# Kernel tuning notes

Hardware: AMD Instinct MI355X
Metric: run time of the kernel (lower is better)

Reference implementation:

```python
import jax, jax.numpy as jnp
import numpy as np

T, H, E, K, I = 4096, 1024, 8, 2, 2048
EPS = 1e-5


def setup_inputs() -> dict:
    key = jax.random.key(0)
    ks = jax.random.split(key, 5)
    xavier = jax.nn.initializers.variance_scaling(1.0, 'fan_avg', 'uniform', dtype=jnp.float32)
    return {
        'x': jax.random.normal(ks[0], (T, H), dtype=jnp.float32),
        'scale': jnp.ones((H,), dtype=jnp.float32),
        'gate_kernel': xavier(ks[1], (H, E), jnp.float32),
        'gate_bias': jnp.zeros((E,), dtype=jnp.float32),
        'mlp1_weight': xavier(ks[2], (E, 2 * I, H), jnp.float32),
        'mlp1_bias': jnp.zeros((E, 2 * I), dtype=jnp.float32),
        'mlp2_weight': xavier(ks[3], (E, H, I), jnp.float32),
        'mlp2_bias': jnp.zeros((E, H), dtype=jnp.float32),
    }


def reference(x, scale, gate_kernel, gate_bias, mlp1_weight, mlp1_bias, mlp2_weight, mlp2_bias):
    # RMSNorm in fp32
    t = x.astype(jnp.float32)
    rms = jnp.sqrt(jnp.mean(t * t, axis=-1, keepdims=True) + EPS)
    normed = ((t / rms) * scale).astype(x.dtype)  # [T, H]

    # Gating: top-k experts + softmax over selected logits
    gate_logits = normed @ gate_kernel + gate_bias  # [T, E]
    expert_logits, expert_indices = jax.lax.top_k(gate_logits, K)  # [T, K]
    expert_weights = jax.nn.softmax(expert_logits, axis=-1)  # [T, K]

    # Dense all-expert SwiGLU MLP (faithful to vmap-over-experts original)
    # mlp1_weight: [E, 2I, H] -> mlp1: [E, T, 2I]
    mlp1 = jnp.einsum('td,efd->etf', normed, mlp1_weight) + mlp1_bias[:, None, :]
    gate_part = jnp.minimum(mlp1[..., :I], 7.0)
    linear_part = jnp.clip(mlp1[..., I:], -7.0, 7.0)
    swish_gate = gate_part * jax.nn.sigmoid(1.702 * gate_part)
    activated = swish_gate * (linear_part + 1.0)  # [E, T, I]
    # mlp2_weight: [E, H, I] -> expert_outputs: [T, E, H]
    expert_outputs = (jnp.einsum('eti,ehi->eth', activated, mlp2_weight)
                      + mlp2_bias[:, None, :]).transpose(1, 0, 2)

    # Scatter top-k weights to dense [T, E] and combine
    one_hot = jax.nn.one_hot(expert_indices, E, dtype=expert_outputs.dtype)  # [T, K, E]
    dense_gate_weights = jnp.sum(one_hot * expert_weights[..., None], axis=1)  # [T, E]
    fused = jnp.einsum('teh,te->th', expert_outputs, dense_gate_weights)
    return x + fused
```

## Files before the change

kernel.cpp:

```cpp
#include <hip/hip_runtime.h>
#include <hip/hip_bf16.h>
#include <math.h>

#define T_ 4096
#define H_ 1024
#define E_ 8
#define KTOP 2
#define I_ 2048
#define EPS_ 1e-5f
#define LDST 72

using bf16x8 = __attribute__((ext_vector_type(8))) short;
using f32x4  = __attribute__((ext_vector_type(4))) float;

static __device__ __forceinline__ unsigned short f2bf(float f) {
    union { float f; unsigned int u; } v; v.f = f;
    unsigned int u = v.u;
    u += 0x7fffu + ((u >> 16) & 1u);
    return (unsigned short)(u >> 16);
}

__global__ __launch_bounds__(256) void k_norm_gate(
    const float* __restrict__ x, const float* __restrict__ scale,
    const float* __restrict__ gk, const float* __restrict__ gb,
    unsigned short* __restrict__ normed_bf,
    int* __restrict__ counts, int* __restrict__ tok_list, float* __restrict__ w_list)
{
    int t = blockIdx.x;
    int tid = threadIdx.x;
    int lane = tid & 63, wave = tid >> 6;

    float4 xv = ((const float4*)(x + (size_t)t * H_))[tid];
    float ss = xv.x*xv.x + xv.y*xv.y + xv.z*xv.z + xv.w*xv.w;
    #pragma unroll
    for (int off = 32; off; off >>= 1) ss += __shfl_down(ss, off);

    __shared__ float red[4];
    __shared__ float s_inv;
    if (lane == 0) red[wave] = ss;
    __syncthreads();
    if (tid == 0) {
        float tot = red[0] + red[1] + red[2] + red[3];
        s_inv = 1.0f / sqrtf(tot / (float)H_ + EPS_);
    }
    __syncthreads();
    float inv = s_inv;

    float4 sv = ((const float4*)scale)[tid];
    float nv[4];
    nv[0] = xv.x*inv*sv.x; nv[1] = xv.y*inv*sv.y;
    nv[2] = xv.z*inv*sv.z; nv[3] = xv.w*inv*sv.w;
    ushort4 nb;
    nb.x = f2bf(nv[0]); nb.y = f2bf(nv[1]); nb.z = f2bf(nv[2]); nb.w = f2bf(nv[3]);
    ((ushort4*)(normed_bf + (size_t)t * H_))[tid] = nb;

    float p[E_];
    #pragma unroll
    for (int e = 0; e < E_; e++) p[e] = 0.f;
    int h0 = tid * 4;
    #pragma unroll
    for (int j = 0; j < 4; j++) {
        const float4* g4 = (const float4*)(gk + (size_t)(h0 + j) * E_);
        float4 a = g4[0], b = g4[1];
        float n = nv[j];
        p[0] += n*a.x; p[1] += n*a.y; p[2] += n*a.z; p[3] += n*a.w;
        p[4] += n*b.x; p[5] += n*b.y; p[6] += n*b.z; p[7] += n*b.w;
    }
    __shared__ float pr[E_][4];
    #pragma unroll
    for (int e = 0; e < E_; e++) {
        float v = p[e];
        #pragma unroll
        for (int off = 32; off; off >>= 1) v += __shfl_down(v, off);
        if (lane == 0) pr[e][wave] = v;
    }
    __syncthreads();
    if (tid == 0) {
        float lg[E_];
        #pragma unroll
        for (int e = 0; e < E_; e++)
            lg[e] = pr[e][0] + pr[e][1] + pr[e][2] + pr[e][3] + gb[e];
        int b0 = -1, b1 = -1; float l0 = -1e30f, l1 = -1e30f;
        #pragma unroll
        for (int e = 0; e < E_; e++) {
            if (lg[e] > l0) { l1 = l0; b1 = b0; l0 = lg[e]; b0 = e; }
            else if (lg[e] > l1) { l1 = lg[e]; b1 = e; }
        }
        float e1 = expf(l1 - l0);
        float w0 = 1.f / (1.f + e1);
        float w1 = e1 / (1.f + e1);
        int p0 = atomicAdd(&counts[b0], 1);
        tok_list[b0 * T_ + p0] = t * 2 + 0; w_list[b0 * T_ + p0] = w0;
        int p1 = atomicAdd(&counts[b1], 1);
        tok_list[b1 * T_ + p1] = t * 2 + 1; w_list[b1 * T_ + p1] = w1;
    }
}

__global__ __launch_bounds__(256) void k_init_out(
    const float* __restrict__ x, float* __restrict__ out)
{
    size_t i = (size_t)blockIdx.x * 256 + threadIdx.x;
    ((float4*)out)[i] = ((const float4*)x)[i];
}

__global__ __launch_bounds__(256) void k_mlp1(
    const float* __restrict__ w1, const float* __restrict__ b1,
    const unsigned short* __restrict__ normed_bf,
    const int* __restrict__ counts, const int* __restrict__ tok_list,
    unsigned short* __restrict__ act)
{
    int e = blockIdx.z;
    int Ne = counts[e];
    int mt0 = blockIdx.y * 64;
    if (mt0 >= Ne) return;
    int it0 = blockIdx.x * 64;
    int tid = threadIdx.x;
    int lane = tid & 63, wave = tid >> 6;
    int quad = lane >> 4, m16 = lane & 15;

    __shared__ unsigned short lA[64 * LDST];
    __shared__ unsigned short lBg[64 * LDST];
    __shared__ unsigned short lBl[64 * LDST];
    __shared__ int ls_tk[64];

    if (tid < 64) {
        int slot = mt0 + tid;
        ls_tk[tid] = (slot < Ne) ? tok_list[e * T_ + slot] : -1;
    }
    __syncthreads();

    f32x4 accg[4], accl[4];
    #pragma unroll
    for (int ns = 0; ns < 4; ns++) {
        accg[ns] = (f32x4){0.f, 0.f, 0.f, 0.f};
        accl[ns] = (f32x4){0.f, 0.f, 0.f, 0.f};
    }

    const size_t w1base = (size_t)e * 2 * I_ * H_;
    int rA = tid >> 3, sgA = tid & 7;
    int nB = tid >> 2, sgB = tid & 3;

    for (int kk = 0; kk < H_; kk += 64) {
        #pragma unroll
        for (int rr = 0; rr < 64; rr += 32) {
            int r = rA + rr;
            int tk = ls_tk[r];
            uint4 v = make_uint4(0u, 0u, 0u, 0u);
            if (tk >= 0)
                v = *(const uint4*)(normed_bf + (size_t)(tk >> 1) * H_ + kk + sgA * 8);
            *(uint4*)(&lA[r * LDST + sgA * 8]) = v;
        }
        {
            const float* srcg = w1 + w1base + (size_t)(it0 + nB) * H_ + kk + sgB * 16;
            const float* srcl = srcg + (size_t)I_ * H_;
            unsigned short tg[16], tl[16];
            #pragma unroll
            for (int q = 0; q < 4; q++) {
                float4 fg = ((const float4*)srcg)[q];
                float4 fl = ((const float4*)srcl)[q];
                tg[q*4+0] = f2bf(fg.x); tg[q*4+1] = f2bf(fg.y);
                tg[q*4+2] = f2bf(fg.z); tg[q*4+3] = f2bf(fg.w);
                tl[q*4+0] = f2bf(fl.x); tl[q*4+1] = f2bf(fl.y);
                tl[q*4+2] = f2bf(fl.z); tl[q*4+3] = f2bf(fl.w);
            }
            *(uint4*)(&lBg[nB * LDST + sgB * 16])     = *(uint4*)(&tg[0]);
            *(uint4*)(&lBg[nB * LDST + sgB * 16 + 8]) = *(uint4*)(&tg[8]);
            *(uint4*)(&lBl[nB * LDST + sgB * 16])     = *(uint4*)(&tl[0]);
            *(uint4*)(&lBl[nB * LDST + sgB * 16 + 8]) = *(uint4*)(&tl[8]);
        }
        __syncthreads();
        #pragma unroll
        for (int ks = 0; ks < 64; ks += 32) {
            bf16x8 af = *(const bf16x8*)(&lA[(wave * 16 + m16) * LDST + ks + quad * 8]);
            #pragma unroll
            for (int ns = 0; ns < 4; ns++) {
                bf16x8 bg = *(const bf16x8*)(&lBg[(ns * 16 + m16) * LDST + ks + quad * 8]);
                accg[ns] = __builtin_amdgcn_mfma_f32_16x16x32_bf16(af, bg, accg[ns], 0, 0, 0);
                bf16x8 bl = *(const bf16x8*)(&lBl[(ns * 16 + m16) * LDST + ks + quad * 8]);
                accl[ns] = __builtin_amdgcn_mfma_f32_16x16x32_bf16(af, bl, accl[ns], 0, 0, 0);
            }
        }
        __syncthreads();
    }

    #pragma unroll
    for (int reg = 0; reg < 4; reg++) {
        int row = wave * 16 + quad * 4 + reg;
        int tk = ls_tk[row];
        if (tk < 0) continue;
        #pragma unroll
        for (int ns = 0; ns < 4; ns++) {
            int i = it0 + ns * 16 + m16;
            float g = accg[ns][reg] + b1[(size_t)e * 2 * I_ + i];
            float l = accl[ns][reg] + b1[(size_t)e * 2 * I_ + I_ + i];
            g = fminf(g, 7.f);
            l = fminf(fmaxf(l, -7.f), 7.f);
            float sw = g / (1.f + expf(-1.702f * g));
            float a = sw * (l + 1.f);
            act[(size_t)tk * I_ + i] = f2bf(a);
        }
    }
}

__global__ __launch_bounds__(256) void k_mlp2(
    const float* __restrict__ w2, const float* __restrict__ b2,
    const unsigned short* __restrict__ act,
    const int* __restrict__ counts, const int* __restrict__ tok_list,
    const float* __restrict__ w_list,
    float* __restrict__ out)
{
    int e = blockIdx.z;
    int Ne = counts[e];
    int mt0 = blockIdx.y * 64;
    if (mt0 >= Ne) return;
    int ht0 = blockIdx.x * 64;
    int tid = threadIdx.x;
    int lane = tid & 63, wave = tid >> 6;
    int quad = lane >> 4, m16 = lane & 15;

    __shared__ unsigned short lA[64 * LDST];
    __shared__ unsigned short lB[64 * LDST];
    __shared__ int ls_tk[64];
    __shared__ float ls_w[64];

    if (tid < 64) {
        int slot = mt0 + tid;
        ls_tk[tid] = (slot < Ne) ? tok_list[e * T_ + slot] : -1;
        ls_w[tid]  = (slot < Ne) ? w_list[e * T_ + slot] : 0.f;
    }
    __syncthreads();

    f32x4 acc[4];
    #pragma unroll
    for (int ns = 0; ns < 4; ns++) acc[ns] = (f32x4){0.f, 0.f, 0.f, 0.f};

    const size_t w2base = (size_t)e * H_ * I_;
    int rA = tid >> 3, sgA = tid & 7;
    int nB = tid >> 2, sgB = tid & 3;

    for (int kk = 0; kk < I_; kk += 64) {
        #pragma unroll
        for (int rr = 0; rr < 64; rr += 32) {
            int r = rA + rr;
            int tk = ls_tk[r];
            uint4 v = make_uint4(0u, 0u, 0u, 0u);
            if (tk >= 0)
                v = *(const uint4*)(act + (size_t)tk * I_ + kk + sgA * 8);
            *(uint4*)(&lA[r * LDST + sgA * 8]) = v;
        }
        {
            const float* src = w2 + w2base + (size_t)(ht0 + nB) * I_ + kk + sgB * 16;
            unsigned short tb[16];
            #pragma unroll
            for (int q = 0; q < 4; q++) {
                float4 f4 = ((const float4*)src)[q];
                tb[q*4+0] = f2bf(f4.x); tb[q*4+1] = f2bf(f4.y);
                tb[q*4+2] = f2bf(f4.z); tb[q*4+3] = f2bf(f4.w);
            }
            *(uint4*)(&lB[nB * LDST + sgB * 16])     = *(uint4*)(&tb[0]);
            *(uint4*)(&lB[nB * LDST + sgB * 16 + 8]) = *(uint4*)(&tb[8]);
        }
        __syncthreads();
        #pragma unroll
        for (int ks = 0; ks < 64; ks += 32) {
            bf16x8 af = *(const bf16x8*)(&lA[(wave * 16 + m16) * LDST + ks + quad * 8]);
            #pragma unroll
            for (int ns = 0; ns < 4; ns++) {
                bf16x8 bf = *(const bf16x8*)(&lB[(ns * 16 + m16) * LDST + ks + quad * 8]);
                acc[ns] = __builtin_amdgcn_mfma_f32_16x16x32_bf16(af, bf, acc[ns], 0, 0, 0);
            }
        }
        __syncthreads();
    }

    #pragma unroll
    for (int reg = 0; reg < 4; reg++) {
        int row = wave * 16 + quad * 4 + reg;
        int tk = ls_tk[row];
        if (tk < 0) continue;
        int t = tk >> 1;
        float wgt = ls_w[row];
        #pragma unroll
        for (int ns = 0; ns < 4; ns++) {
            int h = ht0 + ns * 16 + m16;
            float v = acc[ns][reg] + b2[(size_t)e * H_ + h];
            atomicAdd(&out[(size_t)t * H_ + h], wgt * v);
        }
    }
}

extern "C" void kernel_launch(void* const* d_in, const int* in_sizes, int n_in,
                              void* d_out, int out_size, void* d_ws, size_t ws_size,
                              hipStream_t stream) {
    const float* x     = (const float*)d_in[0];
    const float* scale = (const float*)d_in[1];
    const float* gk    = (const float*)d_in[2];
    const float* gb    = (const float*)d_in[3];
    const float* w1    = (const float*)d_in[4];
    const float* b1    = (const float*)d_in[5];
    const float* w2    = (const float*)d_in[6];
    const float* b2    = (const float*)d_in[7];
    float* out = (float*)d_out;

    char* ws = (char*)d_ws;
    unsigned short* normed_bf = (unsigned short*)ws;
    unsigned short* act       = (unsigned short*)(ws + (size_t)8*1024*1024);
    char* ctl                 = ws + (size_t)40*1024*1024;
    int*   counts   = (int*)ctl;
    int*   tok_list = (int*)(ctl + 256);
    float* w_list   = (float*)(ctl + 256 + (size_t)E_*T_*4);

    hipMemsetAsync(counts, 0, E_ * sizeof(int), stream);

    k_norm_gate<<<dim3(T_), dim3(256), 0, stream>>>(x, scale, gk, gb,
                                                    normed_bf, counts, tok_list, w_list);
    k_init_out<<<dim3(T_ * H_ / (256 * 4)), dim3(256), 0, stream>>>(x, out);
    k_mlp1<<<dim3(I_ / 64, T_ / 64, E_), dim3(256), 0, stream>>>(w1, b1, normed_bf,
                                                                 counts, tok_list, act);
    k_mlp2<<<dim3(H_ / 64, T_ / 64, E_), dim3(256), 0, stream>>>(w2, b2, act,
                                                                 counts, tok_list, w_list, out);
}
```

Measured before the change: 672.8 us.

## Use 128x128 MFMA tiles with bf16 weight pre-conversion and direct global-to-LDS loads

```diff
diff --git a/kernel.cpp b/kernel.cpp
--- a/kernel.cpp
+++ b/kernel.cpp
@@ -8,7 +8,6 @@
 #define KTOP 2
 #define I_ 2048
 #define EPS_ 1e-5f
-#define LDST 72
 
 using bf16x8 = __attribute__((ext_vector_type(8))) short;
 using f32x4  = __attribute__((ext_vector_type(4))) float;
@@ -18,6 +17,25 @@
     unsigned int u = v.u;
     u += 0x7fffu + ((u >> 16) & 1u);
     return (unsigned short)(u >> 16);
+}
+
+static __device__ __forceinline__ void gl_lds16(const void* g, void* l) {
+    __builtin_amdgcn_global_load_lds(
+        (const __attribute__((address_space(1))) unsigned int*)g,
+        (__attribute__((address_space(3))) unsigned int*)l, 16, 0, 0);
+}
+
+__global__ __launch_bounds__(256) void k_convert(
+    const float* __restrict__ src, unsigned short* __restrict__ dst)
+{
+    size_t i = (size_t)blockIdx.x * 256 + threadIdx.x;
+    const float4* s = (const float4*)src + i * 2;
+    float4 a = s[0], b = s[1];
+    ushort4 lo, hi;
+    lo.x = f2bf(a.x); lo.y = f2bf(a.y); lo.z = f2bf(a.z); lo.w = f2bf(a.w);
+    hi.x = f2bf(b.x); hi.y = f2bf(b.y); hi.z = f2bf(b.z); hi.w = f2bf(b.w);
+    ((ushort4*)dst)[i * 2]     = lo;
+    ((ushort4*)dst)[i * 2 + 1] = hi;
 }
 
 __global__ __launch_bounds__(256) void k_norm_gate(
@@ -103,107 +121,169 @@
     ((float4*)out)[i] = ((const float4*)x)[i];
 }
 
+template<bool PRE>
 __global__ __launch_bounds__(256) void k_mlp1(
-    const float* __restrict__ w1, const float* __restrict__ b1,
+    const float* __restrict__ w1f, const unsigned short* __restrict__ w1b,
+    const float* __restrict__ b1,
     const unsigned short* __restrict__ normed_bf,
     const int* __restrict__ counts, const int* __restrict__ tok_list,
     unsigned short* __restrict__ act)
 {
     int e = blockIdx.z;
     int Ne = counts[e];
-    int mt0 = blockIdx.y * 64;
+    int mt0 = blockIdx.y * 128;
     if (mt0 >= Ne) return;
     int it0 = blockIdx.x * 64;
+
     int tid = threadIdx.x;
-    int lane = tid & 63, wave = tid >> 6;
+    int w = tid >> 6, lane = tid & 63;
     int quad = lane >> 4, m16 = lane & 15;
-
-    __shared__ unsigned short lA[64 * LDST];
-    __shared__ unsigned short lBg[64 * LDST];
-    __shared__ unsigned short lBl[64 * LDST];
-    __shared__ int ls_tk[64];
-
-    if (tid < 64) {
+    int wr = w >> 1, wc = w & 1;
+
+    __shared__ __align__(16) char smem[35840];
+    unsigned short* lA = (unsigned short*)smem;
+    unsigned short* lB = (unsigned short*)(smem + 16384);
+    __shared__ int ls_tk[128];
+
+    if (tid < 128) {
         int slot = mt0 + tid;
         ls_tk[tid] = (slot < Ne) ? tok_list[e * T_ + slot] : -1;
     }
     __syncthreads();
 
-    f32x4 accg[4], accl[4];
-    #pragma unroll
-    for (int ns = 0; ns < 4; ns++) {
-        accg[ns] = (f32x4){0.f, 0.f, 0.f, 0.f};
-        accl[ns] = (f32x4){0.f, 0.f, 0.f, 0.f};
-    }
-
-    const size_t w1base = (size_t)e * 2 * I_ * H_;
-    int rA = tid >> 3, sgA = tid & 7;
-    int nB = tid >> 2, sgB = tid & 3;
+    int rsub = lane >> 3, jj = lane & 7;
+    const unsigned short* srcA[4];
+    const unsigned short* srcB[4];
+    const float* srcBf[4];
+    int rowB[4];
+    #pragma unroll
+    for (int c = 0; c < 4; c++) {
+        int r = w * 32 + c * 8 + rsub;
+        int j = jj ^ (r & 7);
+        int tk = ls_tk[r];
+        int tok = (tk < 0) ? 0 : (tk >> 1);
+        srcA[c] = normed_bf + (size_t)tok * H_ + j * 8;
+        int feat = (r < 64) ? (it0 + r) : (I_ + it0 + r - 64);
+        rowB[c] = feat;
+        if (PRE) srcB[c] = w1b + (size_t)e * 2 * I_ * H_ + (size_t)feat * H_ + j * 8;
+    }
+    int rF = tid >> 1, halfF = tid & 1;
+    int featF = (rF < 64) ? (it0 + rF) : (I_ + it0 + rF - 64);
+    if (!PRE) srcBf[0] = w1f + (size_t)e * 2 * I_ * H_ + (size_t)featF * H_ + halfF * 32;
+
+    int aoff[2][4], boff[2][4];
+    #pragma unroll
+    for (int ks2 = 0; ks2 < 2; ks2++) {
+        #pragma unroll
+        for (int i4 = 0; i4 < 4; i4++) {
+            int j = ks2 * 4 + quad;
+            int rA = wr * 64 + i4 * 16 + m16;
+            aoff[ks2][i4] = rA * 64 + ((j ^ (rA & 7)) * 8);
+            int rB = wc * 64 + i4 * 16 + m16;
+            boff[ks2][i4] = rB * 64 + ((j ^ (rB & 7)) * 8);
+        }
+    }
+
+    f32x4 acc[4][4];
+    #pragma unroll
+    for (int mi = 0; mi < 4; mi++)
+        #pragma unroll
+        for (int ni = 0; ni < 4; ni++)
+            acc[mi][ni] = (f32x4){0.f, 0.f, 0.f, 0.f};
 
     for (int kk = 0; kk < H_; kk += 64) {
         #pragma unroll
-        for (int rr = 0; rr < 64; rr += 32) {
-            int r = rA + rr;
-            int tk = ls_tk[r];
-            uint4 v = make_uint4(0u, 0u, 0u, 0u);
-            if (tk >= 0)
-                v = *(const uint4*)(normed_bf + (size_t)(tk >> 1) * H_ + kk + sgA * 8);
-            *(uint4*)(&lA[r * LDST + sgA * 8]) = v;
-        }
-        {
-            const float* srcg = w1 + w1base + (size_t)(it0 + nB) * H_ + kk + sgB * 16;
-            const float* srcl = srcg + (size_t)I_ * H_;
-            unsigned short tg[16], tl[16];
+        for (int c = 0; c < 4; c++) {
+            gl_lds16(srcA[c], lA + (w * 32 + c * 8) * 64);
+            srcA[c] += 64;
+        }
+        if (PRE) {
+            #pragma unroll
+            for (int c = 0; c < 4; c++) {
+                gl_lds16(srcB[c], lB + (w * 32 + c * 8) * 64);
+                srcB[c] += 64;
+            }
+        } else {
+            const float* s = srcBf[0] + kk;
             #pragma unroll
             for (int q = 0; q < 4; q++) {
-                float4 fg = ((const float4*)srcg)[q];
-                float4 fl = ((const float4*)srcl)[q];
-                tg[q*4+0] = f2bf(fg.x); tg[q*4+1] = f2bf(fg.y);
-                tg[q*4+2] = f2bf(fg.z); tg[q*4+3] = f2bf(fg.w);
-                tl[q*4+0] = f2bf(fl.x); tl[q*4+1] = f2bf(fl.y);
-                tl[q*4+2] = f2bf(fl.z); tl[q*4+3] = f2bf(fl.w);
-            }
-            *(uint4*)(&lBg[nB * LDST + sgB * 16])     = *(uint4*)(&tg[0]);
-            *(uint4*)(&lBg[nB * LDST + sgB * 16 + 8]) = *(uint4*)(&tg[8]);
-            *(uint4*)(&lBl[nB * LDST + sgB * 16])     = *(uint4*)(&tl[0]);
-            *(uint4*)(&lBl[nB * LDST + sgB * 16 + 8]) = *(uint4*)(&tl[8]);
+                float4 f0 = ((const float4*)s)[q * 2];
+                float4 f1 = ((const float4*)s)[q * 2 + 1];
+                ushort4 u0, u1;
+                u0.x = f2bf(f0.x); u0.y = f2bf(f0.y); u0.z = f2bf(f0.z); u0.w = f2bf(f0.w);
+                u1.x = f2bf(f1.x); u1.y = f2bf(f1.y); u1.z = f2bf(f1.z); u1.w = f2bf(f1.w);
+                int j = (halfF * 4 + q) ^ (rF & 7);
+                *(ushort4*)(lB + rF * 64 + j * 8)     = u0;
+                *(ushort4*)(lB + rF * 64 + j * 8 + 4) = u1;
+            }
         }
         __syncthreads();
         #pragma unroll
-        for (int ks = 0; ks < 64; ks += 32) {
-            bf16x8 af = *(const bf16x8*)(&lA[(wave * 16 + m16) * LDST + ks + quad * 8]);
-            #pragma unroll
-            for (int ns = 0; ns < 4; ns++) {
-                bf16x8 bg = *(const bf16x8*)(&lBg[(ns * 16 + m16) * LDST + ks + quad * 8]);
-                accg[ns] = __builtin_amdgcn_mfma_f32_16x16x32_bf16(af, bg, accg[ns], 0, 0, 0);
-                bf16x8 bl = *(const bf16x8*)(&lBl[(ns * 16 + m16) * LDST + ks + quad * 8]);
-                accl[ns] = __builtin_amdgcn_mfma_f32_16x16x32_bf16(af, bl, accl[ns], 0, 0, 0);
-            }
+        for (int ks2 = 0; ks2 < 2; ks2++) {
+            bf16x8 av[4], bv[4];
+            #pragma unroll
+            for (int i4 = 0; i4 < 4; i4++) av[i4] = *(const bf16x8*)(lA + aoff[ks2][i4]);
+            #pragma unroll
+            for (int i4 = 0; i4 < 4; i4++) bv[i4] = *(const bf16x8*)(lB + boff[ks2][i4]);
+            #pragma unroll
+            for (int mi = 0; mi < 4; mi++)
+                #pragma unroll
+                for (int ni = 0; ni < 4; ni++)
+                    acc[mi][ni] = __builtin_amdgcn_mfma_f32_16x16x32_bf16(
+                        av[mi], bv[ni], acc[mi][ni], 0, 0, 0);
         }
         __syncthreads();
     }
 
-    #pragma unroll
-    for (int reg = 0; reg < 4; reg++) {
-        int row = wave * 16 + quad * 4 + reg;
-        int tk = ls_tk[row];
-        if (tk < 0) continue;
-        #pragma unroll
-        for (int ns = 0; ns < 4; ns++) {
-            int i = it0 + ns * 16 + m16;
-            float g = accg[ns][reg] + b1[(size_t)e * 2 * I_ + i];
-            float l = accl[ns][reg] + b1[(size_t)e * 2 * I_ + I_ + i];
-            g = fminf(g, 7.f);
-            l = fminf(fmaxf(l, -7.f), 7.f);
-            float sw = g / (1.f + expf(-1.702f * g));
-            float a = sw * (l + 1.f);
-            act[(size_t)tk * I_ + i] = f2bf(a);
-        }
-    }
-}
-
+    float* exL = (float*)smem;
+    float* exG = exL + 4352;
+    const float* b1g = b1 + (size_t)e * 2 * I_;
+    const float* b1l = b1g + I_;
+
+    #pragma unroll
+    for (int mih = 0; mih < 2; mih++) {
+        #pragma unroll
+        for (int ni = 0; ni < 4; ni++) {
+            #pragma unroll
+            for (int reg = 0; reg < 4; reg++) {
+                int ix = (((wr * 2 + mih) * 4 + ni) * 4 + reg) * 68 + quad * 17 + m16;
+                if (wc == 1) exL[ix] = acc[mih][ni][reg];
+                else         exG[ix] = acc[2 + mih][ni][reg];
+            }
+        }
+    }
+    __syncthreads();
+
+    int miBase = (wc == 0) ? 0 : 2;
+    #pragma unroll
+    for (int mih = 0; mih < 2; mih++) {
+        int mi = miBase + mih;
+        #pragma unroll
+        for (int reg = 0; reg < 4; reg++) {
+            int row = wr * 64 + mi * 16 + quad * 4 + reg;
+            int tk = ls_tk[row];
+            if (tk < 0) continue;
+            #pragma unroll
+            for (int ni = 0; ni < 4; ni++) {
+                int i = it0 + ni * 16 + m16;
+                int ix = (((wr * 2 + mih) * 4 + ni) * 4 + reg) * 68 + quad * 17 + m16;
+                float g, l;
+                if (wc == 0) { g = acc[mi][ni][reg]; l = exL[ix]; }
+                else         { g = exG[ix];          l = acc[mi][ni][reg]; }
+                g += b1g[i]; l += b1l[i];
+                g = fminf(g, 7.f);
+                l = fminf(fmaxf(l, -7.f), 7.f);
+                float sw = g / (1.f + expf(-1.702f * g));
+                act[(size_t)tk * I_ + i] = f2bf(sw * (l + 1.f));
+            }
+        }
+    }
+}
+
+template<bool PRE>
 __global__ __launch_bounds__(256) void k_mlp2(
-    const float* __restrict__ w2, const float* __restrict__ b2,
+    const float* __restrict__ w2f, const unsigned short* __restrict__ w2b,
+    const float* __restrict__ b2,
     const unsigned short* __restrict__ act,
     const int* __restrict__ counts, const int* __restrict__ tok_list,
     const float* __restrict__ w_list,
@@ -211,80 +291,124 @@
 {
     int e = blockIdx.z;
     int Ne = counts[e];
-    int mt0 = blockIdx.y * 64;
+    int mt0 = blockIdx.y * 128;
     if (mt0 >= Ne) return;
-    int ht0 = blockIdx.x * 64;
+    int ht0 = blockIdx.x * 128;
+
     int tid = threadIdx.x;
-    int lane = tid & 63, wave = tid >> 6;
+    int w = tid >> 6, lane = tid & 63;
     int quad = lane >> 4, m16 = lane & 15;
-
-    __shared__ unsigned short lA[64 * LDST];
-    __shared__ unsigned short lB[64 * LDST];
-    __shared__ int ls_tk[64];
-    __shared__ float ls_w[64];
-
-    if (tid < 64) {
+    int wr = w >> 1, wc = w & 1;
+
+    __shared__ __align__(16) char smem[32768];
+    unsigned short* lA = (unsigned short*)smem;
+    unsigned short* lB = (unsigned short*)(smem + 16384);
+    __shared__ int ls_tk[128];
+    __shared__ float ls_w[128];
+
+    if (tid < 128) {
         int slot = mt0 + tid;
         ls_tk[tid] = (slot < Ne) ? tok_list[e * T_ + slot] : -1;
         ls_w[tid]  = (slot < Ne) ? w_list[e * T_ + slot] : 0.f;
     }
     __syncthreads();
 
-    f32x4 acc[4];
-    #pragma unroll
-    for (int ns = 0; ns < 4; ns++) acc[ns] = (f32x4){0.f, 0.f, 0.f, 0.f};
-
-    const size_t w2base = (size_t)e * H_ * I_;
-    int rA = tid >> 3, sgA = tid & 7;
-    int nB = tid >> 2, sgB = tid & 3;
+    int rsub = lane >> 3, jj = lane & 7;
+    const unsigned short* srcA[4];
+    const unsigned short* srcB[4];
+    const float* srcBf0 = nullptr;
+    #pragma unroll
+    for (int c = 0; c < 4; c++) {
+        int r = w * 32 + c * 8 + rsub;
+        int j = jj ^ (r & 7);
+        int tk = ls_tk[r];
+        int tka = (tk < 0) ? 0 : tk;
+        srcA[c] = act + (size_t)tka * I_ + j * 8;
+        if (PRE) srcB[c] = w2b + (size_t)e * H_ * I_ + (size_t)(ht0 + r) * I_ + j * 8;
+    }
+    int rF = tid >> 1, halfF = tid & 1;
+    if (!PRE) srcBf0 = w2f + (size_t)e * H_ * I_ + (size_t)(ht0 + rF) * I_ + halfF * 32;
+
+    int aoff[2][4], boff[2][4];
+    #pragma unroll
+    for (int ks2 = 0; ks2 < 2; ks2++) {
+        #pragma unroll
+        for (int i4 = 0; i4 < 4; i4++) {
+            int j = ks2 * 4 + quad;
+            int rA = wr * 64 + i4 * 16 + m16;
+            aoff[ks2][i4] = rA * 64 + ((j ^ (rA & 7)) * 8);
+            int rB = wc * 64 + i4 * 16 + m16;
+            boff[ks2][i4] = rB * 64 + ((j ^ (rB & 7)) * 8);
+        }
+    }
+
+    f32x4 acc[4][4];
+    #pragma unroll
+    for (int mi = 0; mi < 4; mi++)
+        #pragma unroll
+        for (int ni = 0; ni < 4; ni++)
+            acc[mi][ni] = (f32x4){0.f, 0.f, 0.f, 0.f};
 
     for (int kk = 0; kk < I_; kk += 64) {
         #pragma unroll
-        for (int rr = 0; rr < 64; rr += 32) {
-            int r = rA + rr;
-            int tk = ls_tk[r];
-            uint4 v = make_uint4(0u, 0u, 0u, 0u);
-            if (tk >= 0)
-                v = *(const uint4*)(act + (size_t)tk * I_ + kk + sgA * 8);
-            *(uint4*)(&lA[r * LDST + sgA * 8]) = v;
-        }
-        {
-            const float* src = w2 + w2base + (size_t)(ht0 + nB) * I_ + kk + sgB * 16;
-            unsigned short tb[16];
+        for (int c = 0; c < 4; c++) {
+            gl_lds16(srcA[c], lA + (w * 32 + c * 8) * 64);
+            srcA[c] += 64;
+        }
+        if (PRE) {
+            #pragma unroll
+            for (int c = 0; c < 4; c++) {
+                gl_lds16(srcB[c], lB + (w * 32 + c * 8) * 64);
+                srcB[c] += 64;
+            }
+        } else {
+            const float* s = srcBf0 + kk;
             #pragma unroll
             for (int q = 0; q < 4; q++) {
-                float4 f4 = ((const float4*)src)[q];
-                tb[q*4+0] = f2bf(f4.x); tb[q*4+1] = f2bf(f4.y);
-                tb[q*4+2] = f2bf(f4.z); tb[q*4+3] = f2bf(f4.w);
-            }
-            *(uint4*)(&lB[nB * LDST + sgB * 16])     = *(uint4*)(&tb[0]);
-            *(uint4*)(&lB[nB * LDST + sgB * 16 + 8]) = *(uint4*)(&tb[8]);
+                float4 f0 = ((const float4*)s)[q * 2];
+                float4 f1 = ((const float4*)s)[q * 2 + 1];
+                ushort4 u0, u1;
+                u0.x = f2bf(f0.x); u0.y = f2bf(f0.y); u0.z = f2bf(f0.z); u0.w = f2bf(f0.w);
+                u1.x = f2bf(f1.x); u1.y = f2bf(f1.y); u1.z = f2bf(f1.z); u1.w = f2bf(f1.w);
+                int j = (halfF * 4 + q) ^ (rF & 7);
+                *(ushort4*)(lB + rF * 64 + j * 8)     = u0;
+                *(ushort4*)(lB + rF * 64 + j * 8 + 4) = u1;
+            }
         }
         __syncthreads();
         #pragma unroll
-        for (int ks = 0; ks < 64; ks += 32) {
-            bf16x8 af = *(const bf16x8*)(&lA[(wave * 16 + m16) * LDST + ks + quad * 8]);
-            #pragma unroll
-            for (int ns = 0; ns < 4; ns++) {
-                bf16x8 bf = *(const bf16x8*)(&lB[(ns * 16 + m16) * LDST + ks + quad * 8]);
-                acc[ns] = __builtin_amdgcn_mfma_f32_16x16x32_bf16(af, bf, acc[ns], 0, 0, 0);
-            }
+        for (int ks2 = 0; ks2 < 2; ks2++) {
+            bf16x8 av[4], bv[4];
+            #pragma unroll
+            for (int i4 = 0; i4 < 4; i4++) av[i4] = *(const bf16x8*)(lA + aoff[ks2][i4]);
+            #pragma unroll
+            for (int i4 = 0; i4 < 4; i4++) bv[i4] = *(const bf16x8*)(lB + boff[ks2][i4]);
+            #pragma unroll
+            for (int mi = 0; mi < 4; mi++)
+                #pragma unroll
+                for (int ni = 0; ni < 4; ni++)
+                    acc[mi][ni] = __builtin_amdgcn_mfma_f32_16x16x32_bf16(
+                        av[mi], bv[ni], acc[mi][ni], 0, 0, 0);
         }
         __syncthreads();
     }
 
-    #pragma unroll
-    for (int reg = 0; reg < 4; reg++) {
-        int row = wave * 16 + quad * 4 + reg;
-        int tk = ls_tk[row];
-        if (tk < 0) continue;
-        int t = tk >> 1;
-        float wgt = ls_w[row];
-        #pragma unroll
-        for (int ns = 0; ns < 4; ns++) {
-            int h = ht0 + ns * 16 + m16;
-            float v = acc[ns][reg] + b2[(size_t)e * H_ + h];
-            atomicAdd(&out[(size_t)t * H_ + h], wgt * v);
+    const float* b2e = b2 + (size_t)e * H_;
+    #pragma unroll
+    for (int mi = 0; mi < 4; mi++) {
+        #pragma unroll
+        for (int reg = 0; reg < 4; reg++) {
+            int row = wr * 64 + mi * 16 + quad * 4 + reg;
+            int tk = ls_tk[row];
+            if (tk < 0) continue;
+            int t = tk >> 1;
+            float wgt = ls_w[row];
+            #pragma unroll
+            for (int ni = 0; ni < 4; ni++) {
+                int h = ht0 + wc * 64 + ni * 16 + m16;
+                float v = acc[mi][ni][reg] + b2e[h];
+                atomicAdd(&out[(size_t)t * H_ + h], wgt * v);
+            }
         }
     }
 }
@@ -303,20 +427,44 @@
     float* out = (float*)d_out;
 
     char* ws = (char*)d_ws;
+    const size_t MB = 1024 * 1024;
+    bool pre = ws_size >= (size_t)138 * MB;
+
     unsigned short* normed_bf = (unsigned short*)ws;
-    unsigned short* act       = (unsigned short*)(ws + (size_t)8*1024*1024);
-    char* ctl                 = ws + (size_t)40*1024*1024;
+    unsigned short* act       = (unsigned short*)(ws + 8 * MB);
+    unsigned short* w1b = nullptr;
+    unsigned short* w2b = nullptr;
+    char* ctl;
+    if (pre) {
+        w1b = (unsigned short*)(ws + 40 * MB);
+        w2b = (unsigned short*)(ws + 104 * MB);
+        ctl = ws + 136 * MB;
+    } else {
+        ctl = ws + 40 * MB;
+    }
     int*   counts   = (int*)ctl;
     int*   tok_list = (int*)(ctl + 256);
-    float* w_list   = (float*)(ctl + 256 + (size_t)E_*T_*4);
+    float* w_list   = (float*)(ctl + 256 + (size_t)E_ * T_ * 4);
 
     hipMemsetAsync(counts, 0, E_ * sizeof(int), stream);
 
     k_norm_gate<<<dim3(T_), dim3(256), 0, stream>>>(x, scale, gk, gb,
                                                     normed_bf, counts, tok_list, w_list);
+    if (pre) {
+        k_convert<<<dim3((E_ * 2 * I_ * H_) / (256 * 8)), dim3(256), 0, stream>>>(w1, w1b);
+        k_convert<<<dim3((E_ * H_ * I_) / (256 * 8), 1, 1), dim3(256), 0, stream>>>(w2, w2b);
+    }
     k_init_out<<<dim3(T_ * H_ / (256 * 4)), dim3(256), 0, stream>>>(x, out);
-    k_mlp1<<<dim3(I_ / 64, T_ / 64, E_), dim3(256), 0, stream>>>(w1, b1, normed_bf,
-                                                                 counts, tok_list, act);
-    k_mlp2<<<dim3(H_ / 64, T_ / 64, E_), dim3(256), 0, stream>>>(w2, b2, act,
-                                                                 counts, tok_list, w_list, out);
-}
+
+    if (pre) {
+        k_mlp1<true><<<dim3(I_ / 64, T_ / 128, E_), dim3(256), 0, stream>>>(
+            nullptr, w1b, b1, normed_bf, counts, tok_list, act);
+        k_mlp2<true><<<dim3(H_ / 128, T_ / 128, E_), dim3(256), 0, stream>>>(
+            nullptr, w2b, b2, act, counts, tok_list, w_list, out);
+    } else {
+        k_mlp1<false><<<dim3(I_ / 64, T_ / 128, E_), dim3(256), 0, stream>>>(
+            w1, nullptr, b1, normed_bf, counts, tok_list, act);
+        k_mlp2<false><<<dim3(H_ / 128, T_ / 128, E_), dim3(256), 0, stream>>>(
+            w2, nullptr, b2, act, counts, tok_list, w_list, out);
+    }
+}
```

Result: slower. 1.016 ms (+51.0%).
